# Kernel tuning notes

Hardware: AMD Instinct MI355X
Metric: run time of the kernel (lower is better)

The kernel has to match this reference:

```python
import jax, jax.numpy as jnp
import numpy as np

B, N, DIM = 4, 1024, 768
H, GP = 12, 64
HD = DIM // H
SCALE = HD ** -0.5


def setup_inputs() -> dict:
    key = jax.random.key(0)
    ks = jax.random.split(key, 7)
    s = DIM ** -0.5
    return {
        "x": jax.random.normal(ks[0], (B, N, DIM), dtype=jnp.float32),
        "W_qkv": jax.random.normal(ks[1], (3 * DIM, DIM), dtype=jnp.float32) * s,
        "b_qkv": jnp.zeros((3 * DIM,), dtype=jnp.float32),
        "W_gp": jax.random.normal(ks[2], (GP, DIM), dtype=jnp.float32) * s,
        "alpha": jax.random.normal(ks[3], (1, H, 1, 1), dtype=jnp.float32),
        "W_proj": jax.random.normal(ks[4], (DIM, DIM), dtype=jnp.float32) * s,
        "b_proj": jnp.zeros((DIM,), dtype=jnp.float32),
    }


def reference(x, W_qkv, b_qkv, W_gp, alpha, W_proj, b_proj):
    b, n, c = x.shape
    # qkv projection, split into heads: [b, h, n, hd]
    qkv = x @ W_qkv.T + b_qkv
    q, k, v = jnp.split(qkv, 3, axis=-1)
    def to_heads(t):
        return t.reshape(b, n, H, HD).transpose(0, 2, 1, 3)
    q, k, v = to_heads(q), to_heads(k), to_heads(v)

    # raw attention scores [b, h, n, n]
    attn = jnp.einsum('bhnd,bhmd->bhnm', q, k) * SCALE

    # group similarity: gp weight viewed as [h, gp, hd]
    gp = W_gp.reshape(H, GP, HD)
    gw = jnp.einsum('bhnd,hmd->bhnm', v, gp)          # [b, h, n, gp]
    gw = jax.nn.gelu(gw, approximate=False)           # exact GELU (torch default)
    gw = jax.nn.softmax(gw, axis=-1)
    G = jnp.einsum('bhnm,bhkm->bhnk', gw, gw)         # [b, h, n, n]

    # gated combination
    attn = jax.nn.softmax(attn * G, axis=-1)
    a = jax.nn.sigmoid(alpha)                          # [1, h, 1, 1]
    A = (1.0 - a) * attn + a * G
    # column-sum renormalization (sum over query dim 2)
    A = A / (A.sum(axis=2, keepdims=True) + 1e-8)

    out = jnp.einsum('bhnm,bhmd->bhnd', A, v)
    out = out.transpose(0, 2, 1, 3).reshape(b, n, c)
    return out @ W_proj.T + b_proj
```

## Files before the change

### kernel.cpp

```cpp
#include <hip/hip_runtime.h>
#include <math.h>

namespace {

constexpr int kN   = 1024;
constexpr int kDim = 768;
constexpr int kH   = 12;
constexpr int kBH  = 48;
constexpr float kScale = 0.125f;

typedef __attribute__((ext_vector_type(8))) short short8;
typedef __attribute__((ext_vector_type(4))) short short4v;
typedef __attribute__((ext_vector_type(4))) float f32x4;
typedef __attribute__((ext_vector_type(16))) float f32x16;
typedef __attribute__((ext_vector_type(4))) uint uint4v;

#define MFMA(a, b, c)   __builtin_amdgcn_mfma_f32_16x16x32_bf16(a, b, c, 0, 0, 0)
#define MFMA32(a, b, c) __builtin_amdgcn_mfma_f32_32x32x16_bf16(a, b, c, 0, 0, 0)

__device__ __forceinline__ ushort f2bf(float f) {
  uint u = __builtin_bit_cast(uint, f);
  u += 0x7fffu + ((u >> 16) & 1u);
  return (ushort)(u >> 16);
}
__device__ __forceinline__ float bf2f(ushort h) {
  uint u = ((uint)h) << 16;
  return __builtin_bit_cast(float, u);
}
__device__ __forceinline__ void split8(const float* f, short8& hi, short8& lo) {
  #pragma unroll
  for (int i = 0; i < 8; i++) {
    const ushort h = f2bf(f[i]);
    hi[i] = (short)h;
    lo[i] = (short)f2bf(f[i] - bf2f(h));
  }
}
__device__ __forceinline__ uint packbf(float a, float b) {
  return (uint)f2bf(a) | ((uint)f2bf(b) << 16);
}

__device__ __forceinline__ void gl16(const short* g, short* l) {
  __builtin_amdgcn_global_load_lds(
      (const __attribute__((address_space(1))) void*)g,
      (__attribute__((address_space(3))) void*)l, 16, 0, 0);
}

__device__ __forceinline__ short8 frag(const short* t, int row, int chunk) {
  return *(const short8*)(t + row * 64 + ((chunk ^ (row & 7)) << 3));
}

template<int ROWS, int W>
__device__ __forceinline__ void stage_tile(short* dst, const short* src,
                                           int stride, int w, int l) {
  #pragma unroll
  for (int c = 0; c < ROWS / 8; c += W) {
    const int cc = c + w;
    const int row0 = cc << 3;
    const int row = row0 + (l >> 3);
    const int ch = (l & 7) ^ (row & 7);
    gl16(src + (size_t)row * stride + (ch << 3), dst + row0 * 64);
  }
}

__global__ __launch_bounds__(256) void k_split(const float* __restrict__ src,
                                               short* __restrict__ h,
                                               short* __restrict__ l) {
  const size_t i = ((size_t)blockIdx.x * 256 + threadIdx.x) * 4;
  const float4 f = *(const float4*)(src + i);
  const float ff[4] = {f.x, f.y, f.z, f.w};
  short4v hv, lv;
  #pragma unroll
  for (int j = 0; j < 4; j++) {
    const ushort u = f2bf(ff[j]);
    hv[j] = (short)u;
    lv[j] = (short)f2bf(ff[j] - bf2f(u));
  }
  *(short4v*)(h + i) = hv;
  *(short4v*)(l + i) = lv;
}

__global__ __launch_bounds__(512) void k_qkv(const short* __restrict__ xh,
                                             const short* __restrict__ xl,
                                             const short* __restrict__ wh,
                                             const short* __restrict__ wl,
                                             const float* __restrict__ bias,
                                             short* __restrict__ qh, short* __restrict__ ql,
                                             short* __restrict__ kh, short* __restrict__ kl,
                                             short* __restrict__ vh, short* __restrict__ vl) {
  __shared__ __align__(16) short sb[2][32768];
  const int bx = blockIdx.x, by = blockIdx.y;
  const int tid = threadIdx.x, w = tid >> 6, lane = tid & 63;
  const int wr = w >> 2, wc = w & 3;
  const short* Asrc_h = xh + (size_t)(by * 128) * kDim;
  const short* Asrc_l = xl + (size_t)(by * 128) * kDim;
  const short* Bsrc_h = wh + (size_t)(bx * 128) * kDim;
  const short* Bsrc_l = wl + (size_t)(bx * 128) * kDim;

  f32x4 acc[4][2] = {};
  {
    short* nb = sb[0];
    stage_tile<128, 8>(nb,          Asrc_h, kDim, w, lane);
    stage_tile<128, 8>(nb + 8192,   Asrc_l, kDim, w, lane);
    stage_tile<128, 8>(nb + 16384,  Bsrc_h, kDim, w, lane);
    stage_tile<128, 8>(nb + 24576,  Bsrc_l, kDim, w, lane);
  }
  int p = 0;
  #pragma unroll 1
  for (int t = 0; t < 12; ++t) {
    __syncthreads();
    if (t < 11) {
      const int k0 = (t + 1) * 64;
      short* nb = sb[p ^ 1];
      stage_tile<128, 8>(nb,         Asrc_h + k0, kDim, w, lane);
      stage_tile<128, 8>(nb + 8192,  Asrc_l + k0, kDim, w, lane);
      stage_tile<128, 8>(nb + 16384, Bsrc_h + k0, kDim, w, lane);
      stage_tile<128, 8>(nb + 24576, Bsrc_l + k0, kDim, w, lane);
    }
    const short* cb = sb[p];
    #pragma unroll
    for (int s = 0; s < 2; ++s) {
      const int ch = (s << 2) + (lane >> 4);
      short8 af[4], alf[4], bf_[2], blf[2];
      #pragma unroll
      for (int i = 0; i < 4; i++) {
        const int ar = wr * 64 + i * 16 + (lane & 15);
        af[i]  = frag(cb, ar, ch);
        alf[i] = frag(cb + 8192, ar, ch);
      }
      #pragma unroll
      for (int j = 0; j < 2; j++) {
        const int br = wc * 32 + j * 16 + (lane & 15);
        bf_[j] = frag(cb + 16384, br, ch);
        blf[j] = frag(cb + 24576, br, ch);
      }
      #pragma unroll
      for (int i = 0; i < 4; i++)
        #pragma unroll
        for (int j = 0; j < 2; j++) {
          acc[i][j] = MFMA(af[i], bf_[j], acc[i][j]);
          acc[i][j] = MFMA(af[i], blf[j], acc[i][j]);
          acc[i][j] = MFMA(alf[i], bf_[j], acc[i][j]);
        }
    }
    p ^= 1;
  }
  #pragma unroll
  for (int j = 0; j < 2; j++) {
    const int col = bx * 128 + wc * 32 + j * 16 + (lane & 15);
    const int part = col / 768;
    const int rem = col - part * 768;
    const int hh = rem >> 6, d = rem & 63;
    short* dh = (part == 0) ? qh : ((part == 1) ? kh : vh);
    short* dl = (part == 0) ? ql : ((part == 1) ? kl : vl);
    const float bv = bias[col];
    const float scl = (part == 0) ? kScale : 1.0f;
    #pragma unroll
    for (int i = 0; i < 4; i++) {
      #pragma unroll
      for (int r = 0; r < 4; r++) {
        const int gr = by * 128 + wr * 64 + i * 16 + ((lane >> 4) << 2) + r;
        const int b = gr >> 10, n = gr & 1023;
        const float val = (acc[i][j][r] + bv) * scl;
        const ushort hu = f2bf(val);
        const size_t idx = (size_t)((b * kH + hh) * kN + n) * 64 + d;
        dh[idx] = (short)hu;
        dl[idx] = (short)f2bf(val - bf2f(hu));
      }
    }
  }
}

__global__ __launch_bounds__(512) void k_gw(const short* __restrict__ vh,
                                            const short* __restrict__ vl,
                                            const float* __restrict__ Wgp,
                                            short* __restrict__ gwh,
                                            short* __restrict__ gwl) {
  const int bh = blockIdx.x;
  const int h = bh % kH;
  const int n0 = blockIdx.y << 7;
  const int tid = threadIdx.x, w = tid >> 6, lane = tid & 63;
  __shared__ __align__(16) short gph[4096], gpl[4096];
  {
    const int r = tid >> 3, c = tid & 7;
    float f[8] __attribute__((aligned(16)));
    *(float4*)(f + 0) = *(const float4*)(Wgp + h * 4096 + r * 64 + c * 8);
    *(float4*)(f + 4) = *(const float4*)(Wgp + h * 4096 + r * 64 + c * 8 + 4);
    short8 hh, ll;
    split8(f, hh, ll);
    const int slot = c ^ (r & 7);
    *(short8*)(gph + r * 64 + slot * 8) = hh;
    *(short8*)(gpl + r * 64 + slot * 8) = ll;
  }
  short8 vhf[2], vlf[2];
  const size_t arow = (size_t)(bh * kN + n0 + w * 16 + (lane & 15)) * 64 + ((lane >> 4) << 3);
  vhf[0] = *(const short8*)(vh + arow); vhf[1] = *(const short8*)(vh + arow + 32);
  vlf[0] = *(const short8*)(vl + arow); vlf[1] = *(const short8*)(vl + arow + 32);
  __syncthreads();

  f32x4 aU[4] = {};
  #pragma unroll
  for (int msub = 0; msub < 4; msub++) {
    #pragma unroll
    for (int s = 0; s < 2; s++) {
      const int row = (msub << 4) + (lane & 15);
      const int ch = (s << 2) + (lane >> 4);
      const short8 bh_ = frag(gph, row, ch);
      const short8 bl_ = frag(gpl, row, ch);
      aU[msub] = MFMA(vhf[s], bh_, aU[msub]);
      aU[msub] = MFMA(vhf[s], bl_, aU[msub]);
      aU[msub] = MFMA(vlf[s], bh_, aU[msub]);
    }
  }
  #pragma unroll
  for (int r = 0; r < 4; r++) {
    float u[4];
    #pragma unroll
    for (int m = 0; m < 4; m++) {
      const float a = aU[m][r];
      u[m] = 0.5f * a * (1.0f + erff(a * 0.70710678118654752f));
    }
    float mx = fmaxf(fmaxf(u[0], u[1]), fmaxf(u[2], u[3]));
    #pragma unroll
    for (int msk = 1; msk < 16; msk <<= 1) mx = fmaxf(mx, __shfl_xor(mx, msk));
    float e[4], ssum = 0.f;
    #pragma unroll
    for (int m = 0; m < 4; m++) { e[m] = __expf(u[m] - mx); ssum += e[m]; }
    #pragma unroll
    for (int msk = 1; msk < 16; msk <<= 1) ssum += __shfl_xor(ssum, msk);
    const float inv = 1.0f / ssum;
    const int n = n0 + w * 16 + ((lane >> 4) << 2) + r;
    #pragma unroll
    for (int m = 0; m < 4; m++) {
      const float g = e[m] * inv;
      const ushort hu = f2bf(g);
      const size_t idx = (size_t)(bh * kN + n) * 64 + (m << 4) + (lane & 15);
      gwh[idx] = (short)hu;
      gwl[idx] = (short)f2bf(g - bf2f(hu));
    }
  }
}

__global__ __launch_bounds__(256) void k_vt(const short* __restrict__ vh,
                                            const float* __restrict__ rcolv,
                                            short* __restrict__ vtg) {
  const int bh = blockIdx.x;
  const int n0 = blockIdx.y << 6;
  __shared__ short t[64][80];
  const int tid = threadIdx.x;
  {
    const int n = tid >> 2, d0 = (tid & 3) << 4;
    const float rc = rcolv[bh * kN + n0 + n];
    const short8 a = *(const short8*)(vh + (size_t)(bh * kN + n0 + n) * 64 + d0);
    const short8 b = *(const short8*)(vh + (size_t)(bh * kN + n0 + n) * 64 + d0 + 8);
    #pragma unroll
    for (int i = 0; i < 8; ++i) {
      t[d0 + i][n]     = (short)f2bf(bf2f((ushort)a[i]) * rc);
      t[d0 + 8 + i][n] = (short)f2bf(bf2f((ushort)b[i]) * rc);
    }
  }
  __syncthreads();
  const int d = tid >> 2, j0 = (tid & 3) << 4;
  short* dst = vtg + (size_t)bh * 65536 + (size_t)d * 1024 + n0 + j0;
  *(short8*)(dst)     = *(const short8*)(&t[d][j0]);
  *(short8*)(dst + 8) = *(const short8*)(&t[d][j0 + 8]);
}

__global__ __launch_bounds__(256, 3) void k_denom(const short* __restrict__ qh,
                                                  const short* __restrict__ ql,
                                                  const short* __restrict__ kh,
                                                  const short* __restrict__ kl,
                                                  const short* __restrict__ gwh,
                                                  const short* __restrict__ gwl,
                                                  float* __restrict__ rdenom) {
  const int bh = blockIdx.x;
  const int n0 = blockIdx.y << 6;
  const int tid = threadIdx.x, w = tid >> 6, lane = tid & 63;
  const int lc = lane & 31, hl = lane >> 5;
  const int nw = w & 1, mh = w >> 1;
  __shared__ __align__(16) short sb[16384];
  __shared__ float part[4][32];

  short8 qB[4], qlB[4], gB[4], glB[4];
  {
    const size_t nrow = (size_t)(bh * kN + n0 + nw * 32 + lc) * 64;
    #pragma unroll
    for (int ks = 0; ks < 4; ks++) {
      const int off = ks * 16 + (hl << 3);
      qB[ks]  = *(const short8*)(qh  + nrow + off);
      qlB[ks] = *(const short8*)(ql  + nrow + off);
      gB[ks]  = *(const short8*)(gwh + nrow + off);
      glB[ks] = *(const short8*)(gwl + nrow + off);
    }
  }
  float dsum = 0.f;
  #pragma unroll 1
  for (int t = 0; t < 16; ++t) {
    __syncthreads();
    const size_t mo0 = (size_t)(bh * kN + t * 32) * 64;
    const size_t mo1 = (size_t)(bh * kN + 512 + t * 32) * 64;
    stage_tile<32, 4>(sb,                kh  + mo0, 64, w, lane);
    stage_tile<32, 4>(sb + 2048,         kh  + mo1, 64, w, lane);
    stage_tile<32, 4>(sb + 4096,         kl  + mo0, 64, w, lane);
    stage_tile<32, 4>(sb + 4096 + 2048,  kl  + mo1, 64, w, lane);
    stage_tile<32, 4>(sb + 8192,         gwh + mo0, 64, w, lane);
    stage_tile<32, 4>(sb + 8192 + 2048,  gwh + mo1, 64, w, lane);
    stage_tile<32, 4>(sb + 12288,        gwl + mo0, 64, w, lane);
    stage_tile<32, 4>(sb + 12288 + 2048, gwl + mo1, 64, w, lane);
    __syncthreads();
    f32x16 aS = {}, aG = {};
    #pragma unroll
    for (int ks = 0; ks < 4; ++ks) {
      const int row = mh * 32 + lc;
      const int ck = ks * 2 + hl;
      const short8 Ah_ = frag(sb, row, ck);
      const short8 Al_ = frag(sb + 4096, row, ck);
      const short8 Eh_ = frag(sb + 8192, row, ck);
      const short8 El_ = frag(sb + 12288, row, ck);
      aS = MFMA32(Ah_, qB[ks], aS);
      aS = MFMA32(Al_, qB[ks], aS);
      aS = MFMA32(Ah_, qlB[ks], aS);
      aG = MFMA32(Eh_, gB[ks], aG);
      aG = MFMA32(El_, gB[ks], aG);
      aG = MFMA32(Eh_, glB[ks], aG);
    }
    #pragma unroll
    for (int r = 0; r < 16; ++r)
      dsum += __expf(aS[r] * aG[r]);
  }
  dsum += __shfl_xor(dsum, 32);
  if (hl == 0) part[w][lc] = dsum;
  __syncthreads();
  if (tid < 64)
    rdenom[bh * kN + n0 + tid] =
        1.0f / (part[tid >> 5][tid & 31] + part[2 + (tid >> 5)][tid & 31]);
}

__global__ __launch_bounds__(256, 3) void k_colsum(const short* __restrict__ qh,
                                                   const short* __restrict__ ql,
                                                   const short* __restrict__ kh,
                                                   const short* __restrict__ kl,
                                                   const short* __restrict__ gwh,
                                                   const short* __restrict__ gwl,
                                                   const float* __restrict__ rdenom,
                                                   const float* __restrict__ alpha,
                                                   float* __restrict__ rcolv) {
  const int bh = blockIdx.x;
  const int m0 = blockIdx.y << 6;
  const int tid = threadIdx.x, w = tid >> 6, lane = tid & 63;
  const int lc = lane & 31, hl = lane >> 5;
  const int mw = w & 1, nh = w >> 1;
  __shared__ __align__(16) short sb[16384];
  __shared__ float part[4][32];
  __shared__ float rdl[2][32];
  const float ah_ = 1.0f / (1.0f + __expf(-alpha[bh % kH]));
  const float om = 1.0f - ah_;

  short8 kB[4], klB[4], gB[4], glB[4];
  {
    const size_t mrow = (size_t)(bh * kN + m0 + mw * 32 + lc) * 64;
    #pragma unroll
    for (int ks = 0; ks < 4; ks++) {
      const int off = ks * 16 + (hl << 3);
      kB[ks]  = *(const short8*)(kh  + mrow + off);
      klB[ks] = *(const short8*)(kl  + mrow + off);
      gB[ks]  = *(const short8*)(gwh + mrow + off);
      glB[ks] = *(const short8*)(gwl + mrow + off);
    }
  }
  float csum = 0.f;
  #pragma unroll 1
  for (int t = 0; t < 16; ++t) {
    __syncthreads();
    const size_t no0 = (size_t)(bh * kN + t * 32) * 64;
    const size_t no1 = (size_t)(bh * kN + 512 + t * 32) * 64;
    stage_tile<32, 4>(sb,                qh  + no0, 64, w, lane);
    stage_tile<32, 4>(sb + 2048,         qh  + no1, 64, w, lane);
    stage_tile<32, 4>(sb + 4096,         ql  + no0, 64, w, lane);
    stage_tile<32, 4>(sb + 4096 + 2048,  ql  + no1, 64, w, lane);
    stage_tile<32, 4>(sb + 8192,         gwh + no0, 64, w, lane);
    stage_tile<32, 4>(sb + 8192 + 2048,  gwh + no1, 64, w, lane);
    stage_tile<32, 4>(sb + 12288,        gwl + no0, 64, w, lane);
    stage_tile<32, 4>(sb + 12288 + 2048, gwl + no1, 64, w, lane);
    if (tid < 64)
      rdl[tid >> 5][tid & 31] =
          rdenom[bh * kN + (tid >> 5) * 512 + t * 32 + (tid & 31)];
    __syncthreads();
    f32x16 aS = {}, aG = {};
    #pragma unroll
    for (int ks = 0; ks < 4; ++ks) {
      const int row = nh * 32 + lc;
      const int ck = ks * 2 + hl;
      const short8 Ah_ = frag(sb, row, ck);
      const short8 Al_ = frag(sb + 4096, row, ck);
      const short8 Eh_ = frag(sb + 8192, row, ck);
      const short8 El_ = frag(sb + 12288, row, ck);
      aS = MFMA32(Ah_, kB[ks], aS);
      aS = MFMA32(Al_, kB[ks], aS);
      aS = MFMA32(Ah_, klB[ks], aS);
      aG = MFMA32(Eh_, gB[ks], aG);
      aG = MFMA32(El_, gB[ks], aG);
      aG = MFMA32(Eh_, glB[ks], aG);
    }
    #pragma unroll
    for (int r = 0; r < 16; ++r) {
      const int nr = (r & 3) + ((r >> 2) << 3) + (hl << 2);
      const float g = aG[r];
      csum += om * (__expf(aS[r] * g) * rdl[nh][nr]) + ah_ * g;
    }
  }
  csum += __shfl_xor(csum, 32);
  if (hl == 0) part[w][lc] = csum;
  __syncthreads();
  if (tid < 64)
    rcolv[bh * kN + m0 + tid] =
        1.0f / (part[tid >> 5][tid & 31] + part[2 + (tid >> 5)][tid & 31] + 1e-8f);
}

__global__ __launch_bounds__(256, 3) void k_out(const short* __restrict__ qh,
                                                const short* __restrict__ ql,
                                                const short* __restrict__ kh,
                                                const short* __restrict__ kl,
                                                const short* __restrict__ vtg,
                                                const short* __restrict__ gwh,
                                                const short* __restrict__ gwl,
                                                const float* __restrict__ rdenom,
                                                const float* __restrict__ alpha,
                                                short* __restrict__ ctxh,
                                                short* __restrict__ ctxl) {
  const int bh = blockIdx.x;
  const int h = bh % kH;
  const int b = bh / kH;
  const int n0 = blockIdx.y << 6;
  const int tid = threadIdx.x, w = tid >> 6, lane = tid & 63;
  const int lc = lane & 31, hl = lane >> 5;
  const int nw = w & 1, mh = w >> 1;
  __shared__ __align__(16) short sb[20480];
  const float ah_ = 1.0f / (1.0f + __expf(-alpha[h]));
  const float om = 1.0f - ah_;

  short8 qB[4], qlB[4], gB[4], glB[4];
  {
    const size_t nrow = (size_t)(bh * kN + n0 + nw * 32 + lc) * 64;
    #pragma unroll
    for (int ks = 0; ks < 4; ks++) {
      const int off = ks * 16 + (hl << 3);
      qB[ks]  = *(const short8*)(qh  + nrow + off);
      qlB[ks] = *(const short8*)(ql  + nrow + off);
      gB[ks]  = *(const short8*)(gwh + nrow + off);
      glB[ks] = *(const short8*)(gwl + nrow + off);
    }
  }
  const float rdn = rdenom[bh * kN + n0 + nw * 32 + lc];
  const short* vbh = vtg + (size_t)bh * 65536;
  f32x16 oac[2] = {};

  #pragma unroll 1
  for (int t = 0; t < 16; ++t) {
    __syncthreads();
    const size_t mo0 = (size_t)(bh * kN + t * 32) * 64;
    const size_t mo1 = (size_t)(bh * kN + 512 + t * 32) * 64;
    stage_tile<32, 4>(sb,                kh  + mo0, 64, w, lane);
    stage_tile<32, 4>(sb + 2048,         kh  + mo1, 64, w, lane);
    stage_tile<32, 4>(sb + 4096,         kl  + mo0, 64, w, lane);
    stage_tile<32, 4>(sb + 4096 + 2048,  kl  + mo1, 64, w, lane);
    stage_tile<32, 4>(sb + 8192,         gwh + mo0, 64, w, lane);
    stage_tile<32, 4>(sb + 8192 + 2048,  gwh + mo1, 64, w, lane);
    stage_tile<32, 4>(sb + 12288,        gwl + mo0, 64, w, lane);
    stage_tile<32, 4>(sb + 12288 + 2048, gwl + mo1, 64, w, lane);
    #pragma unroll
    for (int c = 0; c < 8; c += 4) {
      const int cc = c + w;
      const int row0 = cc << 3;
      const int row = row0 + (lane >> 3);
      const int ch = (lane & 7) ^ (row & 7);
      const int mg = ((ch >> 2) ? 512 : 0) + t * 32 + ((ch & 3) << 3);
      gl16(vbh + (size_t)row * 1024 + mg, sb + 16384 + row0 * 64);
    }
    __syncthreads();
    f32x16 aS = {}, aG = {};
    #pragma unroll
    for (int ks = 0; ks < 4; ++ks) {
      const int row = mh * 32 + lc;
      const int ck = ks * 2 + hl;
      const short8 Ah_ = frag(sb, row, ck);
      const short8 Al_ = frag(sb + 4096, row, ck);
      const short8 Eh_ = frag(sb + 8192, row, ck);
      const short8 El_ = frag(sb + 12288, row, ck);
      aS = MFMA32(Ah_, qB[ks], aS);
      aS = MFMA32(Al_, qB[ks], aS);
      aS = MFMA32(Ah_, qlB[ks], aS);
      aG = MFMA32(Eh_, gB[ks], aG);
      aG = MFMA32(El_, gB[ks], aG);
      aG = MFMA32(Eh_, glB[ks], aG);
    }
    float a[16];
    #pragma unroll
    for (int r = 0; r < 16; ++r) {
      const float g = aG[r];
      const float p = __expf(aS[r] * g) * rdn;
      a[r] = om * p + ah_ * g;
    }
    short8 pf[2];
    {
      uint W[8], Ws[8];
      #pragma unroll
      for (int j = 0; j < 8; ++j) W[j] = packbf(a[2 * j], a[2 * j + 1]);
      #pragma unroll
      for (int j = 0; j < 8; ++j) Ws[j] = __shfl_xor(W[j], 32);
      uint4v b0, b1;
      b0[0] = hl ? Ws[2] : W[0];  b0[1] = hl ? Ws[3] : W[1];
      b0[2] = hl ? W[2]  : Ws[0]; b0[3] = hl ? W[3]  : Ws[1];
      b1[0] = hl ? Ws[6] : W[4];  b1[1] = hl ? Ws[7] : W[5];
      b1[2] = hl ? W[6]  : Ws[4]; b1[3] = hl ? W[7]  : Ws[5];
      pf[0] = __builtin_bit_cast(short8, b0);
      pf[1] = __builtin_bit_cast(short8, b1);
    }
    #pragma unroll
    for (int dt = 0; dt < 2; ++dt)
      #pragma unroll
      for (int ks = 0; ks < 2; ++ks) {
        const short8 va = frag(sb + 16384, dt * 32 + lc, mh * 4 + ks * 2 + hl);
        oac[dt] = MFMA32(va, pf[ks], oac[dt]);
      }
  }
  __syncthreads();
  float* buf = (float*)sb;
  if (mh == 1) {
    #pragma unroll
    for (int dt = 0; dt < 2; ++dt)
      #pragma unroll
      for (int r = 0; r < 16; ++r) {
        const int d = dt * 32 + (r & 3) + ((r >> 2) << 3) + (hl << 2);
        buf[(nw * 32 + lc) * 68 + d] = oac[dt][r];
      }
  }
  __syncthreads();
  if (mh == 0) {
    #pragma unroll
    for (int dt = 0; dt < 2; ++dt)
      #pragma unroll
      for (int r = 0; r < 16; ++r) {
        const int d = dt * 32 + (r & 3) + ((r >> 2) << 3) + (hl << 2);
        const int idx = (nw * 32 + lc) * 68 + d;
        buf[idx] = oac[dt][r] + buf[idx];
      }
  }
  __syncthreads();
  {
    const int rowi = tid >> 2;
    const int d0 = (tid & 3) << 4;
    float f[16] __attribute__((aligned(16)));
    #pragma unroll
    for (int j = 0; j < 4; ++j)
      *(float4*)(f + 4 * j) = *(const float4*)(&buf[rowi * 68 + d0 + 4 * j]);
    const int n = n0 + rowi;
    short* dsth = ctxh + (size_t)(b * kN + n) * kDim + h * 64 + d0;
    short* dstl = ctxl + (size_t)(b * kN + n) * kDim + h * 64 + d0;
    #pragma unroll
    for (int g8 = 0; g8 < 2; ++g8) {
      short8 hi, lo;
      split8(f + 8 * g8, hi, lo);
      *(short8*)(dsth + 8 * g8) = hi;
      *(short8*)(dstl + 8 * g8) = lo;
    }
  }
}

__global__ __launch_bounds__(512) void k_proj(const short* __restrict__ ch_,
                                              const short* __restrict__ cl_,
                                              const short* __restrict__ wh,
                                              const short* __restrict__ wl,
                                              const float* __restrict__ bias,
                                              float* __restrict__ out) {
  __shared__ __align__(16) short sb[2][32768];
  const int bx = blockIdx.x, by = blockIdx.y;
  const int tid = threadIdx.x, w = tid >> 6, lane = tid & 63;
  const int wr = w >> 2, wc = w & 3;
  const short* Asrc_h = ch_ + (size_t)(by * 128) * kDim;
  const short* Asrc_l = cl_ + (size_t)(by * 128) * kDim;
  const short* Bsrc_h = wh + (size_t)(bx * 128) * kDim;
  const short* Bsrc_l = wl + (size_t)(bx * 128) * kDim;

  f32x4 acc[4][2] = {};
  {
    short* nb = sb[0];
    stage_tile<128, 8>(nb,         Asrc_h, kDim, w, lane);
    stage_tile<128, 8>(nb + 8192,  Asrc_l, kDim, w, lane);
    stage_tile<128, 8>(nb + 16384, Bsrc_h, kDim, w, lane);
    stage_tile<128, 8>(nb + 24576, Bsrc_l, kDim, w, lane);
  }
  int p = 0;
  #pragma unroll 1
  for (int t = 0; t < 12; ++t) {
    __syncthreads();
    if (t < 11) {
      const int k0 = (t + 1) * 64;
      short* nb = sb[p ^ 1];
      stage_tile<128, 8>(nb,         Asrc_h + k0, kDim, w, lane);
      stage_tile<128, 8>(nb + 8192,  Asrc_l + k0, kDim, w, lane);
      stage_tile<128, 8>(nb + 16384, Bsrc_h + k0, kDim, w, lane);
      stage_tile<128, 8>(nb + 24576, Bsrc_l + k0, kDim, w, lane);
    }
    const short* cb = sb[p];
    #pragma unroll
    for (int s = 0; s < 2; ++s) {
      const int ch = (s << 2) + (lane >> 4);
      short8 af[4], alf[4], bf_[2], blf[2];
      #pragma unroll
      for (int i = 0; i < 4; i++) {
        const int ar = wr * 64 + i * 16 + (lane & 15);
        af[i]  = frag(cb, ar, ch);
        alf[i] = frag(cb + 8192, ar, ch);
      }
      #pragma unroll
      for (int j = 0; j < 2; j++) {
        const int br = wc * 32 + j * 16 + (lane & 15);
        bf_[j] = frag(cb + 16384, br, ch);
        blf[j] = frag(cb + 24576, br, ch);
      }
      #pragma unroll
      for (int i = 0; i < 4; i++)
        #pragma unroll
        for (int j = 0; j < 2; j++) {
          acc[i][j] = MFMA(af[i], bf_[j], acc[i][j]);
          acc[i][j] = MFMA(af[i], blf[j], acc[i][j]);
          acc[i][j] = MFMA(alf[i], bf_[j], acc[i][j]);
          acc[i][j] = MFMA(alf[i], blf[j], acc[i][j]);
        }
    }
    p ^= 1;
  }
  #pragma unroll
  for (int j = 0; j < 2; j++) {
    const int col = bx * 128 + wc * 32 + j * 16 + (lane & 15);
    const float bv = bias[col];
    #pragma unroll
    for (int i = 0; i < 4; i++) {
      #pragma unroll
      for (int r = 0; r < 4; r++) {
        const int row = by * 128 + wr * 64 + i * 16 + ((lane >> 4) << 2) + r;
        out[(size_t)row * kDim + col] = acc[i][j][r] + bv;
      }
    }
  }
}

}

extern "C" void kernel_launch(void* const* d_in, const int* in_sizes, int n_in,
                              void* d_out, int out_size, void* d_ws, size_t ws_size,
                              hipStream_t stream) {
  const float* x     = (const float*)d_in[0];
  const float* Wqkv  = (const float*)d_in[1];
  const float* bqkv  = (const float*)d_in[2];
  const float* Wgp   = (const float*)d_in[3];
  const float* alpha = (const float*)d_in[4];
  const float* Wproj = (const float*)d_in[5];
  const float* bproj = (const float*)d_in[6];
  float* out = (float*)d_out;

  const size_t he = 3145728;
  short* qh  = (short*)d_ws;
  short* ql  = qh + he;
  short* kh  = ql + he;
  short* kl  = kh + he;
  short* vh  = kl + he;
  short* vl  = vh + he;
  short* gwh = vl + he;
  short* gwl = gwh + he;
  short* xh  = gwl + he;
  short* xl  = xh + he;
  float* rdenom = (float*)(xl + he);
  float* rcolv  = rdenom + (size_t)kBH * kN;

  short* Wqh = gwh;  short* Wql = gwl;
  short* vtg = vl;
  short* ctxh = xh;  short* ctxl = xl;
  short* Wph = qh;   short* Wpl = ql;

  k_split<<<3072, 256, 0, stream>>>(x, xh, xl);
  k_split<<<1728, 256, 0, stream>>>(Wqkv, Wqh, Wql);
  k_qkv  <<<dim3(18, 32), 512, 0, stream>>>(xh, xl, Wqh, Wql, bqkv,
                                            qh, ql, kh, kl, vh, vl);
  k_gw   <<<dim3(kBH, 8), 512, 0, stream>>>(vh, vl, Wgp, gwh, gwl);
  k_denom<<<dim3(kBH, 16), 256, 0, stream>>>(qh, ql, kh, kl, gwh, gwl, rdenom);
  k_colsum<<<dim3(kBH, 16), 256, 0, stream>>>(qh, ql, kh, kl, gwh, gwl,
                                              rdenom, alpha, rcolv);
  k_vt   <<<dim3(kBH, 16), 256, 0, stream>>>(vh, rcolv, vtg);
  k_out  <<<dim3(kBH, 16), 256, 0, stream>>>(qh, ql, kh, kl, vtg, gwh, gwl,
                                             rdenom, alpha, ctxh, ctxl);
  k_split<<<576, 256, 0, stream>>>(Wproj, Wph, Wpl);
  k_proj <<<dim3(6, 32), 512, 0, stream>>>(ctxh, ctxl, Wph, Wpl, bproj, out);
}
```

Baseline: 253.7 us.

## Materialize fp16 attention matrix in colsum and use it for output matmul

When the workspace is large enough, k_colsum now writes the final combined attention values A (before column normalization) to a full [bh, n, m] fp16 buffer. A new k_outA kernel streams that buffer and the fp16 column-scaled V^T through a single fp16 MFMA, so the Q·K and gw·gw products and the exponentials are no longer recomputed in the output kernel. The cost is roughly 100 MB of extra global writes and reads, scattered 2-byte stores in colsum, and reduced precision from storing A and V in fp16 with one MFMA instead of split bf16 hi/lo terms. If the workspace is too small, the old recompute path runs instead.

```diff
diff --git a/kernel.cpp b/kernel.cpp
--- a/kernel.cpp
+++ b/kernel.cpp
@@ -14,9 +14,11 @@
 typedef __attribute__((ext_vector_type(4))) float f32x4;
 typedef __attribute__((ext_vector_type(16))) float f32x16;
 typedef __attribute__((ext_vector_type(4))) uint uint4v;
-
-#define MFMA(a, b, c)   __builtin_amdgcn_mfma_f32_16x16x32_bf16(a, b, c, 0, 0, 0)
-#define MFMA32(a, b, c) __builtin_amdgcn_mfma_f32_32x32x16_bf16(a, b, c, 0, 0, 0)
+typedef _Float16 f16x8 __attribute__((ext_vector_type(8)));
+
+#define MFMA(a, b, c)      __builtin_amdgcn_mfma_f32_16x16x32_bf16(a, b, c, 0, 0, 0)
+#define MFMA32(a, b, c)    __builtin_amdgcn_mfma_f32_32x32x16_bf16(a, b, c, 0, 0, 0)
+#define MFMA32F16(a, b, c) __builtin_amdgcn_mfma_f32_32x32x16_f16(a, b, c, 0, 0, 0)
 
 __device__ __forceinline__ ushort f2bf(float f) {
   uint u = __builtin_bit_cast(uint, f);
@@ -38,8 +40,11 @@
 __device__ __forceinline__ uint packbf(float a, float b) {
   return (uint)f2bf(a) | ((uint)f2bf(b) << 16);
 }
-
-__device__ __forceinline__ void gl16(const short* g, short* l) {
+__device__ __forceinline__ ushort f2h(float f) {
+  return __builtin_bit_cast(ushort, (_Float16)f);
+}
+
+__device__ __forceinline__ void gl16(const void* g, void* l) {
   __builtin_amdgcn_global_load_lds(
       (const __attribute__((address_space(1))) void*)g,
       (__attribute__((address_space(3))) void*)l, 16, 0, 0);
@@ -240,6 +245,7 @@
   }
 }
 
+template<int F16>
 __global__ __launch_bounds__(256) void k_vt(const short* __restrict__ vh,
                                             const float* __restrict__ rcolv,
                                             short* __restrict__ vtg) {
@@ -254,8 +260,10 @@
     const short8 b = *(const short8*)(vh + (size_t)(bh * kN + n0 + n) * 64 + d0 + 8);
     #pragma unroll
     for (int i = 0; i < 8; ++i) {
-      t[d0 + i][n]     = (short)f2bf(bf2f((ushort)a[i]) * rc);
-      t[d0 + 8 + i][n] = (short)f2bf(bf2f((ushort)b[i]) * rc);
+      const float v0 = bf2f((ushort)a[i]) * rc;
+      const float v1 = bf2f((ushort)b[i]) * rc;
+      t[d0 + i][n]     = F16 ? (short)f2h(v0) : (short)f2bf(v0);
+      t[d0 + 8 + i][n] = F16 ? (short)f2h(v1) : (short)f2bf(v1);
     }
   }
   __syncthreads();
@@ -335,6 +343,7 @@
         1.0f / (part[tid >> 5][tid & 31] + part[2 + (tid >> 5)][tid & 31]);
 }
 
+template<int WA>
 __global__ __launch_bounds__(256, 3) void k_colsum(const short* __restrict__ qh,
                                                    const short* __restrict__ ql,
                                                    const short* __restrict__ kh,
@@ -343,7 +352,8 @@
                                                    const short* __restrict__ gwl,
                                                    const float* __restrict__ rdenom,
                                                    const float* __restrict__ alpha,
-                                                   float* __restrict__ rcolv) {
+                                                   float* __restrict__ rcolv,
+                                                   ushort* __restrict__ Ab) {
   const int bh = blockIdx.x;
   const int m0 = blockIdx.y << 6;
   const int tid = threadIdx.x, w = tid >> 6, lane = tid & 63;
@@ -354,10 +364,12 @@
   __shared__ float rdl[2][32];
   const float ah_ = 1.0f / (1.0f + __expf(-alpha[bh % kH]));
   const float om = 1.0f - ah_;
+  const int m_g = m0 + mw * 32 + lc;
+  ushort* Arow = WA ? (Ab + ((size_t)bh << 20) + m_g) : nullptr;
 
   short8 kB[4], klB[4], gB[4], glB[4];
   {
-    const size_t mrow = (size_t)(bh * kN + m0 + mw * 32 + lc) * 64;
+    const size_t mrow = (size_t)(bh * kN + m_g) * 64;
     #pragma unroll
     for (int ks = 0; ks < 4; ks++) {
       const int off = ks * 16 + (hl << 3);
@@ -405,7 +417,12 @@
     for (int r = 0; r < 16; ++r) {
       const int nr = (r & 3) + ((r >> 2) << 3) + (hl << 2);
       const float g = aG[r];
-      csum += om * (__expf(aS[r] * g) * rdl[nh][nr]) + ah_ * g;
+      const float a = om * (__expf(aS[r] * g) * rdl[nh][nr]) + ah_ * g;
+      csum += a;
+      if (WA) {
+        const int n_g = nh * 512 + t * 32 + nr;
+        Arow[(size_t)n_g << 10] = f2h(a);
+      }
     }
   }
   csum += __shfl_xor(csum, 32);
@@ -416,17 +433,102 @@
         1.0f / (part[tid >> 5][tid & 31] + part[2 + (tid >> 5)][tid & 31] + 1e-8f);
 }
 
-__global__ __launch_bounds__(256, 3) void k_out(const short* __restrict__ qh,
-                                                const short* __restrict__ ql,
-                                                const short* __restrict__ kh,
-                                                const short* __restrict__ kl,
-                                                const short* __restrict__ vtg,
-                                                const short* __restrict__ gwh,
-                                                const short* __restrict__ gwl,
-                                                const float* __restrict__ rdenom,
-                                                const float* __restrict__ alpha,
-                                                short* __restrict__ ctxh,
-                                                short* __restrict__ ctxl) {
+__global__ __launch_bounds__(256) void k_outA(const ushort* __restrict__ Ab,
+                                              const short* __restrict__ vtf,
+                                              short* __restrict__ ctxh,
+                                              short* __restrict__ ctxl) {
+  const int bh = blockIdx.x;
+  const int h = bh % kH;
+  const int b = bh / kH;
+  const int n0 = blockIdx.y << 6;
+  const int tid = threadIdx.x, w = tid >> 6, lane = tid & 63;
+  const int lc = lane & 31, hl = lane >> 5;
+  const int nw = w & 1, mh = w >> 1;
+  __shared__ __align__(16) short sbm[10240];
+  short* At = sbm;
+  short* Vt = sbm + 4096;
+  const ushort* Abh = Ab + ((size_t)bh << 20);
+  const short* Vbh = vtf + ((size_t)bh << 16);
+  f32x16 oac[2] = {};
+
+  #pragma unroll 1
+  for (int t = 0; t < 16; ++t) {
+    __syncthreads();
+    #pragma unroll
+    for (int c = 0; c < 8; c += 4) {
+      const int cc = c + w;
+      const int row0 = cc << 3;
+      const int row = row0 + (lane >> 3);
+      const int ce = (lane & 7) ^ (row & 7);
+      const int mg = ((ce >> 2) ? 512 : 0) + t * 32 + ((ce & 3) << 3);
+      gl16(Abh + ((size_t)(n0 + row) << 10) + mg, At + row0 * 64);
+      gl16(Vbh + ((size_t)row << 10) + mg, Vt + row0 * 64);
+    }
+    __syncthreads();
+    #pragma unroll
+    for (int dt = 0; dt < 2; ++dt)
+      #pragma unroll
+      for (int ks = 0; ks < 2; ++ks) {
+        const int ck = mh * 4 + ks * 2 + hl;
+        const f16x8 va = __builtin_bit_cast(f16x8, frag(Vt, dt * 32 + lc, ck));
+        const f16x8 pe = __builtin_bit_cast(f16x8, frag(At, nw * 32 + lc, ck));
+        oac[dt] = MFMA32F16(va, pe, oac[dt]);
+      }
+  }
+  __syncthreads();
+  float* buf = (float*)sbm;
+  if (mh == 1) {
+    #pragma unroll
+    for (int dt = 0; dt < 2; ++dt)
+      #pragma unroll
+      for (int r = 0; r < 16; ++r) {
+        const int d = dt * 32 + (r & 3) + ((r >> 2) << 3) + (hl << 2);
+        buf[(nw * 32 + lc) * 68 + d] = oac[dt][r];
+      }
+  }
+  __syncthreads();
+  if (mh == 0) {
+    #pragma unroll
+    for (int dt = 0; dt < 2; ++dt)
+      #pragma unroll
+      for (int r = 0; r < 16; ++r) {
+        const int d = dt * 32 + (r & 3) + ((r >> 2) << 3) + (hl << 2);
+        const int idx = (nw * 32 + lc) * 68 + d;
+        buf[idx] = oac[dt][r] + buf[idx];
+      }
+  }
+  __syncthreads();
+  {
+    const int rowi = tid >> 2;
+    const int d0 = (tid & 3) << 4;
+    float f[16] __attribute__((aligned(16)));
+    #pragma unroll
+    for (int j = 0; j < 4; ++j)
+      *(float4*)(f + 4 * j) = *(const float4*)(&buf[rowi * 68 + d0 + 4 * j]);
+    const int n = n0 + rowi;
+    short* dsth = ctxh + (size_t)(b * kN + n) * kDim + h * 64 + d0;
+    short* dstl = ctxl + (size_t)(b * kN + n) * kDim + h * 64 + d0;
+    #pragma unroll
+    for (int g8 = 0; g8 < 2; ++g8) {
+      short8 hi, lo;
+      split8(f + 8 * g8, hi, lo);
+      *(short8*)(dsth + 8 * g8) = hi;
+      *(short8*)(dstl + 8 * g8) = lo;
+    }
+  }
+}
+
+__global__ __launch_bounds__(256, 3) void k_out9(const short* __restrict__ qh,
+                                                 const short* __restrict__ ql,
+                                                 const short* __restrict__ kh,
+                                                 const short* __restrict__ kl,
+                                                 const short* __restrict__ vtg,
+                                                 const short* __restrict__ gwh,
+                                                 const short* __restrict__ gwl,
+                                                 const float* __restrict__ rdenom,
+                                                 const float* __restrict__ alpha,
+                                                 short* __restrict__ ctxh,
+                                                 short* __restrict__ ctxl) {
   const int bh = blockIdx.x;
   const int h = bh % kH;
   const int b = bh / kH;
@@ -672,9 +774,13 @@
   short* xl  = xh + he;
   float* rdenom = (float*)(xl + he);
   float* rcolv  = rdenom + (size_t)kBH * kN;
+  ushort* Ab    = (ushort*)(rcolv + (size_t)kBH * kN);
+  const size_t need_mat = (size_t)(rcolv + (size_t)kBH * kN - (float*)d_ws) * 4
+                        + (size_t)kBH * kN * kN * 2;
+  const bool mat = ws_size >= need_mat;
 
   short* Wqh = gwh;  short* Wql = gwl;
-  short* vtg = vl;
+  short* vt  = vl;
   short* ctxh = xh;  short* ctxl = xl;
   short* Wph = qh;   short* Wpl = ql;
 
@@ -684,11 +790,18 @@
                                             qh, ql, kh, kl, vh, vl);
   k_gw   <<<dim3(kBH, 8), 512, 0, stream>>>(vh, vl, Wgp, gwh, gwl);
   k_denom<<<dim3(kBH, 16), 256, 0, stream>>>(qh, ql, kh, kl, gwh, gwl, rdenom);
-  k_colsum<<<dim3(kBH, 16), 256, 0, stream>>>(qh, ql, kh, kl, gwh, gwl,
-                                              rdenom, alpha, rcolv);
-  k_vt   <<<dim3(kBH, 16), 256, 0, stream>>>(vh, rcolv, vtg);
-  k_out  <<<dim3(kBH, 16), 256, 0, stream>>>(qh, ql, kh, kl, vtg, gwh, gwl,
-                                             rdenom, alpha, ctxh, ctxl);
+  if (mat) {
+    k_colsum<1><<<dim3(kBH, 16), 256, 0, stream>>>(qh, ql, kh, kl, gwh, gwl,
+                                                   rdenom, alpha, rcolv, Ab);
+    k_vt<1> <<<dim3(kBH, 16), 256, 0, stream>>>(vh, rcolv, vt);
+    k_outA  <<<dim3(kBH, 16), 256, 0, stream>>>(Ab, vt, ctxh, ctxl);
+  } else {
+    k_colsum<0><<<dim3(kBH, 16), 256, 0, stream>>>(qh, ql, kh, kl, gwh, gwl,
+                                                   rdenom, alpha, rcolv, nullptr);
+    k_vt<0> <<<dim3(kBH, 16), 256, 0, stream>>>(vh, rcolv, vt);
+    k_out9  <<<dim3(kBH, 16), 256, 0, stream>>>(qh, ql, kh, kl, vt, gwh, gwl,
+                                                rdenom, alpha, ctxh, ctxl);
+  }
   k_split<<<576, 256, 0, stream>>>(Wproj, Wph, Wpl);
   k_proj <<<dim3(6, 32), 512, 0, stream>>>(ctxh, ctxl, Wph, Wpl, bproj, out);
 }
```

Result: faster. 225.3 us (-11.2%).
